# Optimization experiments

Hardware: AMD Instinct MI355X
Metric: run time of the kernel (lower is better)

Reference implementation:

```python
import jax, jax.numpy as jnp
import numpy as np

N, IN_F, E, EDGE_F, H, C = 50000, 128, 800000, 32, 4, 32
NEG_SLOPE = 0.2
EPS = 1e-16


def setup_inputs() -> dict:
    key = jax.random.key(0)
    ks = jax.random.split(key, 10)
    s = lambda *sh: 1.0 / np.sqrt(sh[-1])
    return {
        "node_features": jax.random.normal(ks[0], (N, IN_F), jnp.float32),
        "edge_features": jax.random.normal(ks[1], (E, EDGE_F), jnp.float32),
        "edge_index": jax.random.randint(ks[2], (2, E), 0, N, jnp.int32),
        # GATConv params
        "W_gat": jax.random.normal(ks[3], (H * C, IN_F), jnp.float32) * s(IN_F),
        "att_src": jax.random.normal(ks[4], (H, C), jnp.float32) * s(C),
        "att_dst": jax.random.normal(ks[5], (H, C), jnp.float32) * s(C),
        "att_edge": jax.random.normal(ks[6], (H, C), jnp.float32) * s(C),
        "bias": jnp.zeros((H * C,), jnp.float32),
        # edge_linear and skip_connection weights
        "W_edge": jax.random.normal(ks[7], (H * C, EDGE_F), jnp.float32) * s(EDGE_F),
        "W_skip": jax.random.normal(ks[8], (H * C, IN_F), jnp.float32) * s(IN_F),
    }


def reference(node_features, edge_features, edge_index, W_gat, att_src, att_dst,
              att_edge, bias, W_edge, W_skip):
    src, dst = edge_index[0], edge_index[1]
    # edge_linear + view(-1, H, C)
    e_attr = (edge_features @ W_edge.T).reshape(E, H, C)
    # GATConv: per-head linear transform of nodes -> [N, H, C]
    x = (node_features @ W_gat.T).reshape(N, H, C)
    # attention logits: a_src.x_i + a_dst.x_j + a_edge.e  -> [E, H]
    a_src = jnp.einsum('nhc,hc->nh', x, att_src)
    a_dst = jnp.einsum('nhc,hc->nh', x, att_dst)
    a_edge = jnp.einsum('ehc,hc->eh', e_attr, att_edge)
    alpha = jax.nn.leaky_relu(a_src[src] + a_dst[dst] + a_edge, NEG_SLOPE)
    # segment softmax over incoming edges of each destination node
    m = jax.ops.segment_max(alpha, dst, num_segments=N)  # [N, H]
    m = jnp.where(jnp.isfinite(m), m, 0.0)
    ex = jnp.exp(alpha - m[dst])
    denom = jax.ops.segment_sum(ex, dst, num_segments=N)  # [N, H]
    attn = ex / (denom[dst] + EPS)  # [E, H]
    # message = alpha * x_src ; scatter-add to destination
    msg = x[src] * attn[:, :, None]  # [E, H, C]
    out = jax.ops.segment_sum(msg, dst, num_segments=N)  # [N, H, C]
    out = out.reshape(N, H * C) + bias  # concat=True
    # skip connection + ELU activation
    out = out + node_features @ W_skip.T
    return jax.nn.elu(out)
```

## Files before the change

kernel.cpp:

```cpp
#include <hip/hip_runtime.h>
#include <hip/hip_bf16.h>

constexpr int N_NODES = 50000;
constexpr int IN_F    = 128;
constexpr long E_EDGES = 800000;
constexpr int EDGE_F  = 32;
constexpr int H_HEADS = 4;
constexpr int C_CH    = 32;
constexpr int HC      = 128;
constexpr float NEG_SLOPE = 0.2f;
constexpr float EPS = 1e-16f;
constexpr int B_HIST = 64;
constexpr int CHUNK  = (int)(E_EDGES / B_HIST);
constexpr int HWORDS = N_NODES / 2;
constexpr int NB_SCAN = (N_NODES + 255) / 256;
constexpr int NB_EL   = (int)(E_EDGES / 256);
constexpr int NB_AE2  = (int)(E_EDGES / 128);
constexpr float SM_SHIFT = 12.0f;

typedef __attribute__((ext_vector_type(8))) short bf16x8;
typedef __attribute__((ext_vector_type(4))) float f32x4;

__device__ __forceinline__ unsigned short f2b(float f) {
    __hip_bfloat16 h = __float2bfloat16(f);
    return *reinterpret_cast<unsigned short*>(&h);
}
__device__ __forceinline__ float b2f_lo(unsigned v) { return __uint_as_float(v << 16); }
__device__ __forceinline__ float b2f_hi(unsigned v) { return __uint_as_float(v & 0xffff0000u); }

__global__ __launch_bounds__(256) void setup_kernel(
    const float* __restrict__ Wg, const float* __restrict__ Ws,
    unsigned short* __restrict__ wcat, const float* __restrict__ We,
    const float* __restrict__ att_edge, float* __restrict__ weff)
{
    const int b = blockIdx.x, t = threadIdx.x;
    if (b < 32) {
        int i = (b * 256 + t) * 4;
        const float* srcp = (i < 16384) ? (Wg + i) : (Ws + i - 16384);
        float4 v = *(const float4*)srcp;
        ushort4 o;
        o.x = f2b(v.x); o.y = f2b(v.y); o.z = f2b(v.z); o.w = f2b(v.w);
        *(ushort4*)&wcat[i] = o;
    } else {
        if (t < 128) {
            int h = t >> 5, f = t & 31;
            float acc = 0.f;
#pragma unroll
            for (int c = 0; c < C_CH; ++c)
                acc = fmaf(We[(h * C_CH + c) * EDGE_F + f], att_edge[h * C_CH + c], acc);
            weff[t] = acc;
        }
    }
}

__global__ __launch_bounds__(1024) void hist_kernel(
    const int* __restrict__ dst, unsigned int* __restrict__ histB,
    unsigned short* __restrict__ rank16)
{
    __shared__ unsigned int h[HWORDS];
    const int t = threadIdx.x, b = blockIdx.x;
    for (int i = t; i < HWORDS; i += 1024) h[i] = 0;
    __syncthreads();
    const int e0 = b * CHUNK;
    for (int i = t; i < CHUNK; i += 1024) {
        int d = dst[e0 + i];
        int sh = (d & 1) * 16;
        unsigned old = atomicAdd(&h[d >> 1], 1u << sh);
        rank16[e0 + i] = (unsigned short)((old >> sh) & 0xFFFFu);
    }
    __syncthreads();
    unsigned int* outp = histB + (size_t)b * HWORDS;
    for (int i = t; i < HWORDS; i += 1024) outp[i] = h[i];
}

__global__ __launch_bounds__(256) void ae_kernel(
    const float* __restrict__ ef, const float* __restrict__ weff,
    float* __restrict__ ae)
{
    const int t = threadIdx.x;
    const int l = t & 63, wv = t >> 6;
    const int sub = l & 3, eIdx = l >> 2;
    const long eb = (long)blockIdx.x * 128 + wv * 32 + eIdx;
    const float4* ef4 = (const float4*)ef;

    float4 a0 = ef4[eb * 8 + sub];
    float4 b0 = ef4[eb * 8 + 4 + sub];
    float4 a1 = ef4[(eb + 16) * 8 + sub];
    float4 b1 = ef4[(eb + 16) * 8 + 4 + sub];

    const float4* wf4 = (const float4*)weff;
    float4 wa[4], wb[4];
#pragma unroll
    for (int h = 0; h < 4; ++h) { wa[h] = wf4[h * 8 + sub]; wb[h] = wf4[h * 8 + 4 + sub]; }

    float p[4];
#pragma unroll
    for (int h = 0; h < 4; ++h) {
        float acc = 0.f;
        acc = fmaf(a0.x, wa[h].x, acc); acc = fmaf(a0.y, wa[h].y, acc);
        acc = fmaf(a0.z, wa[h].z, acc); acc = fmaf(a0.w, wa[h].w, acc);
        acc = fmaf(b0.x, wb[h].x, acc); acc = fmaf(b0.y, wb[h].y, acc);
        acc = fmaf(b0.z, wb[h].z, acc); acc = fmaf(b0.w, wb[h].w, acc);
        p[h] = acc;
    }
#pragma unroll
    for (int h = 0; h < 4; ++h) {
        p[h] += __shfl_xor(p[h], 1);
        p[h] += __shfl_xor(p[h], 2);
    }
    float v0 = (sub == 0) ? p[0] : (sub == 1) ? p[1] : (sub == 2) ? p[2] : p[3];
    ae[eb * 4 + sub] = v0;

#pragma unroll
    for (int h = 0; h < 4; ++h) {
        float acc = 0.f;
        acc = fmaf(a1.x, wa[h].x, acc); acc = fmaf(a1.y, wa[h].y, acc);
        acc = fmaf(a1.z, wa[h].z, acc); acc = fmaf(a1.w, wa[h].w, acc);
        acc = fmaf(b1.x, wb[h].x, acc); acc = fmaf(b1.y, wb[h].y, acc);
        acc = fmaf(b1.z, wb[h].z, acc); acc = fmaf(b1.w, wb[h].w, acc);
        p[h] = acc;
    }
#pragma unroll
    for (int h = 0; h < 4; ++h) {
        p[h] += __shfl_xor(p[h], 1);
        p[h] += __shfl_xor(p[h], 2);
    }
    float v1 = (sub == 0) ? p[0] : (sub == 1) ? p[1] : (sub == 2) ? p[2] : p[3];
    ae[(eb + 16) * 4 + sub] = v1;
}

__global__ __launch_bounds__(256) void mfma_gemm_kernel(
    const float* __restrict__ nf, const unsigned short* __restrict__ wcat,
    const float* __restrict__ bias, unsigned short* __restrict__ xb,
    float* __restrict__ out)
{
    const int t  = threadIdx.x;
    const int w  = t >> 6;
    const int l  = t & 63;
    const int lr = l & 15;
    const int lk = l >> 4;
    const int n0 = blockIdx.x * 64;

    bf16x8 bfr[4][4];
#pragma unroll
    for (int nfr = 0; nfr < 4; ++nfr)
#pragma unroll
        for (int ks = 0; ks < 4; ++ks)
            bfr[nfr][ks] = *(const bf16x8*)&wcat[(w * 64 + nfr * 16 + lr) * 128 + ks * 32 + lk * 8];

    f32x4 acc[4][4];
#pragma unroll
    for (int mf = 0; mf < 4; ++mf)
#pragma unroll
        for (int nfr = 0; nfr < 4; ++nfr)
            acc[mf][nfr] = (f32x4){0.f, 0.f, 0.f, 0.f};

#pragma unroll
    for (int ks = 0; ks < 4; ++ks) {
        bf16x8 afr[4];
#pragma unroll
        for (int mf = 0; mf < 4; ++mf) {
            int row = n0 + mf * 16 + lr;
            row = row < N_NODES ? row : N_NODES - 1;
            const float* ap = nf + (size_t)row * IN_F + ks * 32 + lk * 8;
            float4 a0 = *(const float4*)ap;
            float4 a1 = *(const float4*)(ap + 4);
            bf16x8 f;
            f[0] = (short)f2b(a0.x); f[1] = (short)f2b(a0.y);
            f[2] = (short)f2b(a0.z); f[3] = (short)f2b(a0.w);
            f[4] = (short)f2b(a1.x); f[5] = (short)f2b(a1.y);
            f[6] = (short)f2b(a1.z); f[7] = (short)f2b(a1.w);
            afr[mf] = f;
        }
#pragma unroll
        for (int mf = 0; mf < 4; ++mf)
#pragma unroll
            for (int nfr = 0; nfr < 4; ++nfr)
                acc[mf][nfr] = __builtin_amdgcn_mfma_f32_16x16x32_bf16(
                    afr[mf], bfr[nfr][ks], acc[mf][nfr], 0, 0, 0);
    }

#pragma unroll
    for (int nfr = 0; nfr < 4; ++nfr) {
        const int gc = w * 64 + nfr * 16 + lr;
        if (gc < HC) {
#pragma unroll
            for (int mf = 0; mf < 4; ++mf)
#pragma unroll
                for (int r = 0; r < 4; ++r) {
                    int m = n0 + mf * 16 + lk * 4 + r;
                    if (m < N_NODES) xb[(size_t)m * HC + gc] = f2b(acc[mf][nfr][r]);
                }
        } else {
            const float bv = bias[gc - HC];
#pragma unroll
            for (int mf = 0; mf < 4; ++mf)
#pragma unroll
                for (int r = 0; r < 4; ++r) {
                    int m = n0 + mf * 16 + lk * 4 + r;
                    if (m < N_NODES) out[(size_t)m * HC + gc - HC] = acc[mf][nfr][r] + bv;
                }
        }
    }
}

__global__ __launch_bounds__(256) void a_kernel(
    const unsigned int* __restrict__ xb32, const float* __restrict__ att_src,
    const float* __restrict__ att_dst, float* __restrict__ asrc,
    float* __restrict__ adst)
{
    const int wave = threadIdx.x >> 6, lane = threadIdx.x & 63;
    const int n = blockIdx.x * 4 + wave;
    if (n >= N_NODES) return;
    unsigned v = xb32[(size_t)n * 64 + lane];
    float x0 = b2f_lo(v), x1 = b2f_hi(v);
    float2 as = ((const float2*)att_src)[lane];
    float2 ad = ((const float2*)att_dst)[lane];
    float ps = x0 * as.x + x1 * as.y;
    float pd = x0 * ad.x + x1 * ad.y;
#pragma unroll
    for (int off = 1; off < 16; off <<= 1) {
        ps += __shfl_xor(ps, off);
        pd += __shfl_xor(pd, off);
    }
    if ((lane & 15) == 0) {
        asrc[(size_t)n * H_HEADS + (lane >> 4)] = ps;
        adst[(size_t)n * H_HEADS + (lane >> 4)] = pd;
    }
}

__global__ __launch_bounds__(256) void scan1_kernel(const unsigned int* __restrict__ histB,
                                                    int* __restrict__ row_ptr,
                                                    int* __restrict__ blocksum)
{
    __shared__ int s[256];
    int t = threadIdx.x;
    int i = blockIdx.x * 256 + t;
    int v = 0;
    if (i < N_NODES) {
        int w = i >> 1, sh = (i & 1) * 16;
#pragma unroll 8
        for (int b = 0; b < B_HIST; ++b)
            v += (int)((histB[(size_t)b * HWORDS + w] >> sh) & 0xFFFFu);
    }
    s[t] = v;
    __syncthreads();
#pragma unroll
    for (int off = 1; off < 256; off <<= 1) {
        int u = (t >= off) ? s[t - off] : 0;
        __syncthreads();
        s[t] += u;
        __syncthreads();
    }
    if (i < N_NODES) row_ptr[i] = s[t] - v;
    if (t == 255) blocksum[blockIdx.x] = s[255];
}

__global__ __launch_bounds__(256) void scan2_kernel(int* __restrict__ blocksum)
{
    __shared__ int s[256];
    int t = threadIdx.x;
    int v = (t < NB_SCAN) ? blocksum[t] : 0;
    s[t] = v;
    __syncthreads();
#pragma unroll
    for (int off = 1; off < 256; off <<= 1) {
        int u = (t >= off) ? s[t - off] : 0;
        __syncthreads();
        s[t] += u;
        __syncthreads();
    }
    blocksum[t] = s[t] - v;
}

__global__ __launch_bounds__(256) void scan3_kernel(int* __restrict__ row_ptr,
                                                    const int* __restrict__ blocksum,
                                                    const unsigned int* __restrict__ histB,
                                                    int* __restrict__ off)
{
    int i = blockIdx.x * 256 + threadIdx.x;
    if (i < N_NODES) {
        int run = row_ptr[i] + blocksum[blockIdx.x];
        row_ptr[i] = run;
        int w = i >> 1, sh = (i & 1) * 16;
#pragma unroll 8
        for (int b = 0; b < B_HIST; ++b) {
            off[(size_t)b * N_NODES + i] = run;
            run += (int)((histB[(size_t)b * HWORDS + w] >> sh) & 0xFFFFu);
        }
    }
    if (i == 0) row_ptr[N_NODES] = (int)E_EDGES;
}

__global__ __launch_bounds__(256) void edge_logits_kernel(
    const int* __restrict__ src, const int* __restrict__ dst,
    const float* __restrict__ ae, const float* __restrict__ asrc,
    const float* __restrict__ adst, const int* __restrict__ off,
    const unsigned short* __restrict__ rank16, uint4* __restrict__ rec4)
{
    const int e = blockIdx.x * 256 + threadIdx.x;

    const int s  = src[e];
    const int d  = dst[e];
    const int rk = (int)rank16[e];
    float4 a_e = ((const float4*)ae)[e];

    float4 as4 = ((const float4*)asrc)[s];
    float4 ad4 = ((const float4*)adst)[d];
    const int be = e / CHUNK;
    const int pos = off[(size_t)be * N_NODES + d] + rk;

    float lg[4] = {as4.x + ad4.x + a_e.x, as4.y + ad4.y + a_e.y,
                   as4.z + ad4.z + a_e.z, as4.w + ad4.w + a_e.w};
    uint4 r;
    unsigned* rw = (unsigned*)&r;
#pragma unroll
    for (int h = 0; h < 4; ++h) {
        float al = lg[h] > 0.f ? lg[h] : NEG_SLOPE * lg[h];
        rw[h] = (__float_as_uint(al) & 0xFFFFFF00u)
              | ((unsigned)(s >> (8 * h)) & 0xFFu);
    }
    rec4[pos] = r;
}

__device__ __forceinline__ void accum8(float* acc, uint4 v, float e) {
    acc[0] = fmaf(b2f_lo(v.x), e, acc[0]);
    acc[1] = fmaf(b2f_hi(v.x), e, acc[1]);
    acc[2] = fmaf(b2f_lo(v.y), e, acc[2]);
    acc[3] = fmaf(b2f_hi(v.y), e, acc[3]);
    acc[4] = fmaf(b2f_lo(v.z), e, acc[4]);
    acc[5] = fmaf(b2f_hi(v.z), e, acc[5]);
    acc[6] = fmaf(b2f_lo(v.w), e, acc[6]);
    acc[7] = fmaf(b2f_hi(v.w), e, acc[7]);
}

__device__ __forceinline__ int rec_src(uint4 r) {
    return (int)((r.x & 0xFFu) | ((r.y & 0xFFu) << 8));
}
__device__ __forceinline__ float rec_alpha(uint4 r, int h) {
    unsigned w = h == 0 ? r.x : h == 1 ? r.y : h == 2 ? r.z : r.w;
    return __uint_as_float(w & 0xFFFFFF00u);
}

__global__ __launch_bounds__(256) void aggregate_kernel(
    const int* __restrict__ row_ptr, const uint4* __restrict__ rec4,
    const uint4* __restrict__ xb4, float* __restrict__ out)
{
    const int wave = threadIdx.x >> 6;
    const int lane = threadIdx.x & 63;
    const int d = blockIdx.x * 4 + wave;
    if (d >= N_NODES) return;
    const int beg = row_ptr[d], end = row_ptr[d + 1];
    const int q  = lane >> 4;
    const int cg = lane & 15;
    const int h  = cg >> 2;

    float acc[8] = {0.f, 0.f, 0.f, 0.f, 0.f, 0.f, 0.f, 0.f};
    float dsum = 0.f;

    int i = beg;
    for (; i + 8 <= end; i += 8) {
        int i0 = i + q, i1 = i + 4 + q;
        uint4 r0 = rec4[i0];
        uint4 r1 = rec4[i1];
        int s0 = rec_src(r0);
        int s1 = rec_src(r1);
        float a0 = rec_alpha(r0, h);
        float a1 = rec_alpha(r1, h);
        uint4 v0 = xb4[(size_t)s0 * 16 + cg];
        uint4 v1 = xb4[(size_t)s1 * 16 + cg];
        float e0 = __expf(a0 - SM_SHIFT);
        float e1 = __expf(a1 - SM_SHIFT);
        dsum += e0 + e1;
        accum8(acc, v0, e0);
        accum8(acc, v1, e1);
    }
    for (; i < end; i += 4) {
        int idx = i + q;
        bool val = idx < end;
        int ii = val ? idx : end - 1;
        uint4 r = rec4[ii];
        int s = rec_src(r);
        float a = rec_alpha(r, h);
        uint4 v = xb4[(size_t)s * 16 + cg];
        float e = val ? __expf(a - SM_SHIFT) : 0.f;
        dsum += e;
        accum8(acc, v, e);
    }

#pragma unroll
    for (int off = 16; off <= 32; off <<= 1) {
        dsum += __shfl_xor(dsum, off);
#pragma unroll
        for (int k = 0; k < 8; ++k) acc[k] += __shfl_xor(acc[k], off);
    }
    const float inv = 1.f / (dsum + EPS);

    if (q == 0) {
        float* op = out + (size_t)d * HC + cg * 8;
        float4 o0 = *(const float4*)op;
        float4 o1 = *(const float4*)(op + 4);
        o0.x += acc[0] * inv; o0.y += acc[1] * inv;
        o0.z += acc[2] * inv; o0.w += acc[3] * inv;
        o1.x += acc[4] * inv; o1.y += acc[5] * inv;
        o1.z += acc[6] * inv; o1.w += acc[7] * inv;
        o0.x = o0.x > 0.f ? o0.x : expf(o0.x) - 1.f;
        o0.y = o0.y > 0.f ? o0.y : expf(o0.y) - 1.f;
        o0.z = o0.z > 0.f ? o0.z : expf(o0.z) - 1.f;
        o0.w = o0.w > 0.f ? o0.w : expf(o0.w) - 1.f;
        o1.x = o1.x > 0.f ? o1.x : expf(o1.x) - 1.f;
        o1.y = o1.y > 0.f ? o1.y : expf(o1.y) - 1.f;
        o1.z = o1.z > 0.f ? o1.z : expf(o1.z) - 1.f;
        o1.w = o1.w > 0.f ? o1.w : expf(o1.w) - 1.f;
        *(float4*)op = o0;
        *(float4*)(op + 4) = o1;
    }
}

extern "C" void kernel_launch(void* const* d_in, const int* in_sizes, int n_in,
                              void* d_out, int out_size, void* d_ws, size_t ws_size,
                              hipStream_t stream)
{
    const float* nf       = (const float*)d_in[0];
    const float* ef       = (const float*)d_in[1];
    const int*   ei       = (const int*)d_in[2];
    const float* Wg       = (const float*)d_in[3];
    const float* att_src  = (const float*)d_in[4];
    const float* att_dst  = (const float*)d_in[5];
    const float* att_edge = (const float*)d_in[6];
    const float* bias     = (const float*)d_in[7];
    const float* We       = (const float*)d_in[8];
    const float* Ws       = (const float*)d_in[9];
    float* out = (float*)d_out;

    const int* src = ei;
    const int* dst = ei + E_EDGES;

    unsigned int* rec   = (unsigned int*)d_ws;
    float* ae           = (float*)(rec + 4 * E_EDGES);
    unsigned short* xb  = (unsigned short*)(ae + 4 * E_EDGES);
    unsigned short* wcat= xb + (size_t)N_NODES * HC;
    float* asrc         = (float*)(wcat + 256 * 128);
    float* adst         = asrc + (size_t)N_NODES * H_HEADS;
    float* weff         = adst + (size_t)N_NODES * H_HEADS;
    unsigned int* histB = (unsigned int*)(weff + 128);
    int*   off          = (int*)(histB + (size_t)B_HIST * HWORDS);
    int*   row_ptr      = off + (size_t)B_HIST * N_NODES;
    int*   blocksum     = row_ptr + N_NODES + 1;
    unsigned short* rank16 = (unsigned short*)(blocksum + 256);

    setup_kernel<<<33, 256, 0, stream>>>(
        Wg, Ws, wcat, We, att_edge, weff);
    hist_kernel<<<B_HIST, 1024, 0, stream>>>(dst, histB, rank16);
    ae_kernel<<<NB_AE2, 256, 0, stream>>>(ef, weff, ae);
    mfma_gemm_kernel<<<(N_NODES + 63) / 64, 256, 0, stream>>>(
        nf, wcat, bias, xb, out);
    a_kernel<<<(N_NODES + 3) / 4, 256, 0, stream>>>(
        (const unsigned int*)xb, att_src, att_dst, asrc, adst);
    scan1_kernel<<<NB_SCAN, 256, 0, stream>>>(histB, row_ptr, blocksum);
    scan2_kernel<<<1, 256, 0, stream>>>(blocksum);
    scan3_kernel<<<NB_SCAN, 256, 0, stream>>>(row_ptr, blocksum, histB, off);
    edge_logits_kernel<<<NB_EL, 256, 0, stream>>>(
        src, dst, ae, asrc, adst, off, rank16, (uint4*)rec);
    aggregate_kernel<<<(N_NODES + 3) / 4, 256, 0, stream>>>(
        row_ptr, (const uint4*)rec, (const uint4*)xb, out);
}
```

Before: 161.8 us.

## Fuse histogram and edge-attention kernels into one launch to run concurrently

Merges the destination histogram/rank kernel and the edge-feature attention projection kernel into a single launch. The first 64 blocks build the histogram and the rest compute edge logits, with each of those blocks now handling 512 edges and bounds checks added. The aim is to keep the rest of the GPU busy while the 64 histogram blocks run, and to save one launch. In exchange, every block now reserves the 100KB shared histogram array, which limits the edge-logit blocks to low occupancy per CU.

```diff
diff --git a/kernel.cpp b/kernel.cpp
--- a/kernel.cpp
+++ b/kernel.cpp
@@ -15,7 +15,7 @@
 constexpr int HWORDS = N_NODES / 2;
 constexpr int NB_SCAN = (N_NODES + 255) / 256;
 constexpr int NB_EL   = (int)(E_EDGES / 256);
-constexpr int NB_AE2  = (int)(E_EDGES / 128);
+constexpr int NB_AE10 = (int)((E_EDGES + 511) / 512);
 constexpr float SM_SHIFT = 12.0f;
 
 typedef __attribute__((ext_vector_type(8))) short bf16x8;
@@ -53,80 +53,81 @@
     }
 }
 
-__global__ __launch_bounds__(1024) void hist_kernel(
+__global__ __launch_bounds__(1024) void hist_ae_kernel(
     const int* __restrict__ dst, unsigned int* __restrict__ histB,
-    unsigned short* __restrict__ rank16)
+    unsigned short* __restrict__ rank16, const float* __restrict__ ef,
+    const float* __restrict__ weff, float* __restrict__ ae)
 {
     __shared__ unsigned int h[HWORDS];
-    const int t = threadIdx.x, b = blockIdx.x;
-    for (int i = t; i < HWORDS; i += 1024) h[i] = 0;
-    __syncthreads();
-    const int e0 = b * CHUNK;
-    for (int i = t; i < CHUNK; i += 1024) {
-        int d = dst[e0 + i];
-        int sh = (d & 1) * 16;
-        unsigned old = atomicAdd(&h[d >> 1], 1u << sh);
-        rank16[e0 + i] = (unsigned short)((old >> sh) & 0xFFFFu);
-    }
-    __syncthreads();
-    unsigned int* outp = histB + (size_t)b * HWORDS;
-    for (int i = t; i < HWORDS; i += 1024) outp[i] = h[i];
-}
-
-__global__ __launch_bounds__(256) void ae_kernel(
-    const float* __restrict__ ef, const float* __restrict__ weff,
-    float* __restrict__ ae)
-{
-    const int t = threadIdx.x;
+    const int b = blockIdx.x, t = threadIdx.x;
+
+    if (b < B_HIST) {
+        for (int i = t; i < HWORDS; i += 1024) h[i] = 0;
+        __syncthreads();
+        const int e0 = b * CHUNK;
+        for (int i = t; i < CHUNK; i += 1024) {
+            int d = dst[e0 + i];
+            int sh = (d & 1) * 16;
+            unsigned old = atomicAdd(&h[d >> 1], 1u << sh);
+            rank16[e0 + i] = (unsigned short)((old >> sh) & 0xFFFFu);
+        }
+        __syncthreads();
+        unsigned int* outp = histB + (size_t)b * HWORDS;
+        for (int i = t; i < HWORDS; i += 1024) outp[i] = h[i];
+        return;
+    }
+
     const int l = t & 63, wv = t >> 6;
     const int sub = l & 3, eIdx = l >> 2;
-    const long eb = (long)blockIdx.x * 128 + wv * 32 + eIdx;
+    const long eb = (long)(b - B_HIST) * 512 + wv * 32 + eIdx;
     const float4* ef4 = (const float4*)ef;
-
-    float4 a0 = ef4[eb * 8 + sub];
-    float4 b0 = ef4[eb * 8 + 4 + sub];
-    float4 a1 = ef4[(eb + 16) * 8 + sub];
-    float4 b1 = ef4[(eb + 16) * 8 + 4 + sub];
-
     const float4* wf4 = (const float4*)weff;
     float4 wa[4], wb[4];
 #pragma unroll
-    for (int h = 0; h < 4; ++h) { wa[h] = wf4[h * 8 + sub]; wb[h] = wf4[h * 8 + 4 + sub]; }
-
-    float p[4];
-#pragma unroll
-    for (int h = 0; h < 4; ++h) {
-        float acc = 0.f;
-        acc = fmaf(a0.x, wa[h].x, acc); acc = fmaf(a0.y, wa[h].y, acc);
-        acc = fmaf(a0.z, wa[h].z, acc); acc = fmaf(a0.w, wa[h].w, acc);
-        acc = fmaf(b0.x, wb[h].x, acc); acc = fmaf(b0.y, wb[h].y, acc);
-        acc = fmaf(b0.z, wb[h].z, acc); acc = fmaf(b0.w, wb[h].w, acc);
-        p[h] = acc;
-    }
-#pragma unroll
-    for (int h = 0; h < 4; ++h) {
-        p[h] += __shfl_xor(p[h], 1);
-        p[h] += __shfl_xor(p[h], 2);
-    }
-    float v0 = (sub == 0) ? p[0] : (sub == 1) ? p[1] : (sub == 2) ? p[2] : p[3];
-    ae[eb * 4 + sub] = v0;
-
-#pragma unroll
-    for (int h = 0; h < 4; ++h) {
-        float acc = 0.f;
-        acc = fmaf(a1.x, wa[h].x, acc); acc = fmaf(a1.y, wa[h].y, acc);
-        acc = fmaf(a1.z, wa[h].z, acc); acc = fmaf(a1.w, wa[h].w, acc);
-        acc = fmaf(b1.x, wb[h].x, acc); acc = fmaf(b1.y, wb[h].y, acc);
-        acc = fmaf(b1.z, wb[h].z, acc); acc = fmaf(b1.w, wb[h].w, acc);
-        p[h] = acc;
-    }
-#pragma unroll
-    for (int h = 0; h < 4; ++h) {
-        p[h] += __shfl_xor(p[h], 1);
-        p[h] += __shfl_xor(p[h], 2);
-    }
-    float v1 = (sub == 0) ? p[0] : (sub == 1) ? p[1] : (sub == 2) ? p[2] : p[3];
-    ae[(eb + 16) * 4 + sub] = v1;
+    for (int hh = 0; hh < 4; ++hh) { wa[hh] = wf4[hh * 8 + sub]; wb[hh] = wf4[hh * 8 + 4 + sub]; }
+
+    if (eb < E_EDGES) {
+        float4 a0 = ef4[eb * 8 + sub];
+        float4 b0 = ef4[eb * 8 + 4 + sub];
+        float p[4];
+#pragma unroll
+        for (int hh = 0; hh < 4; ++hh) {
+            float acc = 0.f;
+            acc = fmaf(a0.x, wa[hh].x, acc); acc = fmaf(a0.y, wa[hh].y, acc);
+            acc = fmaf(a0.z, wa[hh].z, acc); acc = fmaf(a0.w, wa[hh].w, acc);
+            acc = fmaf(b0.x, wb[hh].x, acc); acc = fmaf(b0.y, wb[hh].y, acc);
+            acc = fmaf(b0.z, wb[hh].z, acc); acc = fmaf(b0.w, wb[hh].w, acc);
+            p[hh] = acc;
+        }
+#pragma unroll
+        for (int hh = 0; hh < 4; ++hh) {
+            p[hh] += __shfl_xor(p[hh], 1);
+            p[hh] += __shfl_xor(p[hh], 2);
+        }
+        float v0 = (sub == 0) ? p[0] : (sub == 1) ? p[1] : (sub == 2) ? p[2] : p[3];
+        ae[eb * 4 + sub] = v0;
+    }
+    if (eb + 16 < E_EDGES) {
+        float4 a1 = ef4[(eb + 16) * 8 + sub];
+        float4 b1 = ef4[(eb + 16) * 8 + 4 + sub];
+        float p[4];
+#pragma unroll
+        for (int hh = 0; hh < 4; ++hh) {
+            float acc = 0.f;
+            acc = fmaf(a1.x, wa[hh].x, acc); acc = fmaf(a1.y, wa[hh].y, acc);
+            acc = fmaf(a1.z, wa[hh].z, acc); acc = fmaf(a1.w, wa[hh].w, acc);
+            acc = fmaf(b1.x, wb[hh].x, acc); acc = fmaf(b1.y, wb[hh].y, acc);
+            acc = fmaf(b1.z, wb[hh].z, acc); acc = fmaf(b1.w, wb[hh].w, acc);
+            p[hh] = acc;
+        }
+#pragma unroll
+        for (int hh = 0; hh < 4; ++hh) {
+            p[hh] += __shfl_xor(p[hh], 1);
+            p[hh] += __shfl_xor(p[hh], 2);
+        }
+        float v1 = (sub == 0) ? p[0] : (sub == 1) ? p[1] : (sub == 2) ? p[2] : p[3];
+        ae[(eb + 16) * 4 + sub] = v1;
+    }
 }
 
 __global__ __launch_bounds__(256) void mfma_gemm_kernel(
@@ -451,8 +452,8 @@
 
     setup_kernel<<<33, 256, 0, stream>>>(
         Wg, Ws, wcat, We, att_edge, weff);
-    hist_kernel<<<B_HIST, 1024, 0, stream>>>(dst, histB, rank16);
-    ae_kernel<<<NB_AE2, 256, 0, stream>>>(ef, weff, ae);
+    hist_ae_kernel<<<B_HIST + NB_AE10, 1024, 0, stream>>>(
+        dst, histB, rank16, ef, weff, ae);
     mfma_gemm_kernel<<<(N_NODES + 63) / 64, 256, 0, stream>>>(
         nf, wcat, bias, xb, out);
     a_kernel<<<(N_NODES + 3) / 4, 256, 0, stream>>>(
```

Result: no change. 160.9 us (-0.5%).
